# Kernel optimization log

Measured on AMD Instinct MI355X. Metric: run time of the kernel, lower is better.

## Reference

```python
import jax, jax.numpy as jnp
import numpy as np

EMBED_DIM = 1024
NUM_HEADS = 16
KEY_SIZE = 1024
VALUE_SIZE = 1024
N, L = 4, 2048


def setup_inputs() -> dict:
    key = jax.random.key(0)
    ks = jax.random.split(key, 8)
    s = lambda fan_in: 1.0 / np.sqrt(fan_in)
    return {
        "x": jax.random.normal(ks[0], (N, L, EMBED_DIM), dtype=jnp.float32),
        # nn.Linear weights stored as (out, in); we apply x @ W.T
        "W_q": jax.random.uniform(ks[1], (KEY_SIZE, EMBED_DIM), jnp.float32, -s(EMBED_DIM), s(EMBED_DIM)),
        "W_k": jax.random.uniform(ks[2], (KEY_SIZE, EMBED_DIM), jnp.float32, -s(EMBED_DIM), s(EMBED_DIM)),
        "W_v": jax.random.uniform(ks[3], (VALUE_SIZE, EMBED_DIM), jnp.float32, -s(EMBED_DIM), s(EMBED_DIM)),
        "W_qp": jax.random.uniform(ks[4], (KEY_SIZE, KEY_SIZE), jnp.float32, -s(KEY_SIZE), s(KEY_SIZE)),
        "W_kp": jax.random.uniform(ks[5], (KEY_SIZE, KEY_SIZE), jnp.float32, -s(KEY_SIZE), s(KEY_SIZE)),
        "W_vp": jax.random.uniform(ks[6], (VALUE_SIZE, VALUE_SIZE), jnp.float32, -s(VALUE_SIZE), s(VALUE_SIZE)),
        "W_out": jax.random.uniform(ks[7], (EMBED_DIM, VALUE_SIZE), jnp.float32, -s(VALUE_SIZE), s(VALUE_SIZE)),
    }


def reference(x, W_q, W_k, W_v, W_qp, W_kp, W_vp, W_out):
    H = NUM_HEADS
    q = (x @ W_q.T) @ W_qp.T   # (N, L, key_size)
    k = (x @ W_k.T) @ W_kp.T   # (N, L, key_size)
    v = (x @ W_v.T) @ W_vp.T   # (N, L, value_size)
    n, l, vs = v.shape
    dq = q.shape[-1] // H
    dv = vs // H
    q = q.reshape(n, l, H, dq).transpose(0, 2, 1, 3)  # (N, H, L, dq)
    k = k.reshape(n, l, H, dq).transpose(0, 2, 1, 3)
    v = v.reshape(n, l, H, dv).transpose(0, 2, 1, 3)
    att = jnp.einsum("nhid,nhjd->nhij", q, k) / jnp.sqrt(jnp.float32(dq))
    att = jax.nn.softmax(att, axis=-1)
    out = jnp.einsum("nhij,nhjd->nhid", att, v)       # (N, H, L, dv)
    out = out.transpose(0, 2, 1, 3).reshape(n, l, vs)
    return out @ W_out.T
```

## Files before the change

### kernel.cpp

```cpp
#include <hip/hip_runtime.h>
#include <cstddef>
#include <cstdint>

#define EMBED 1024
#define NH    16
#define DQ    64
#define NB    4
#define LSEQ  2048
#define MROWS (NB * LSEQ)

typedef __bf16 bf16x8 __attribute__((ext_vector_type(8)));
typedef float  f32x4  __attribute__((ext_vector_type(4)));

__device__ __forceinline__ unsigned short f2bf(float f) {
    return (unsigned short)((__float_as_uint(f) + 0x8000u) >> 16);
}

__device__ __forceinline__ unsigned pack2(float a, float b) {
    unsigned ua = __float_as_uint(a) + 0x8000u;
    unsigned ub = __float_as_uint(b) + 0x8000u;
    return __builtin_amdgcn_perm(ub, ua, 0x07060302u);
}

__device__ __forceinline__ uint2 pack4(float a, float b, float c, float d) {
    return make_uint2(pack2(a, b), pack2(c, d));
}

__device__ __forceinline__ unsigned pack2t(float a, float b) {
    return __builtin_amdgcn_perm(__float_as_uint(b), __float_as_uint(a), 0x07060302u);
}

__device__ __forceinline__ uint2 pack4t(float a, float b, float c, float d) {
    return make_uint2(pack2t(a, b), pack2t(c, d));
}

__device__ __forceinline__ void async_cp16(const void* g, void* l) {
    __builtin_amdgcn_global_load_lds((const __attribute__((address_space(1))) unsigned int*)g,
                                     (__attribute__((address_space(3))) unsigned int*)l,
                                     16, 0, 0);
}

struct CvtJobs {
    const float* src[8];
    unsigned short* dst[8];
    int n[8];
};

__global__ __launch_bounds__(256) void cvt_bf16(CvtJobs j) {
    int job = blockIdx.y;
    const float* s = j.src[job];
    unsigned short* d = j.dst[job];
    int n4 = j.n[job] >> 2;
    int stride = gridDim.x * blockDim.x;
    for (int i = blockIdx.x * blockDim.x + threadIdx.x; i < n4; i += stride) {
        float4 f = ((const float4*)s)[i];
        ((uint2*)d)[i] = pack4(f.x, f.y, f.z, f.w);
    }
}

struct TransJobs {
    const float* src[3];
    unsigned short* dst[3];
};

__global__ __launch_bounds__(256) void transpose_cvt(TransJobs tj) {
    __shared__ unsigned short Ts[64][68];
    const float* src = tj.src[blockIdx.z];
    unsigned short* dst = tj.dst[blockIdx.z];
    const int tid = threadIdx.x;
    const int r0 = blockIdx.y * 64;
    const int c0 = blockIdx.x * 64;

    {
        int col4 = tid & 15;
        int rb   = tid >> 4;
#pragma unroll
        for (int it = 0; it < 4; it++) {
            int r = rb + it * 16;
            float4 f = *(const float4*)(src + (size_t)(r0 + r) * 1024 + c0 + col4 * 4);
            *(uint2*)&Ts[r][col4 * 4] = pack4(f.x, f.y, f.z, f.w);
        }
    }
    __syncthreads();

    {
        int oc = tid >> 2;
        int seg = tid & 3;
        __attribute__((aligned(16))) unsigned short tmp[16];
#pragma unroll
        for (int e = 0; e < 16; e++) tmp[e] = Ts[seg * 16 + e][oc];
        unsigned short* out = dst + (size_t)(c0 + oc) * 1024 + r0 + seg * 16;
        *(uint4*)(out)     = *(const uint4*)&tmp[0];
        *(uint4*)(out + 8) = *(const uint4*)&tmp[8];
    }
}

struct BGemmArgs {
    const unsigned short* A[3];
    const unsigned short* B[3];
    void* C[3];
    int mode[3];
    float scl[3];
};

__global__ __launch_bounds__(256) void gemm_bf16nt(BGemmArgs p, int M, int N, int K) {
    __shared__ __align__(16) unsigned short As[128 * 64];
    __shared__ __align__(16) unsigned short Bs[128 * 64];

    const int tid  = threadIdx.x;
    const int wave = tid >> 6;
    const int lane = tid & 63;
    const int m16  = lane & 15;
    const int kq   = lane >> 4;
    const int bm = blockIdx.y * 128;
    const int bn = blockIdx.x * 128;
    const int z  = blockIdx.z;
    const unsigned short* A = p.A[z];
    const unsigned short* B = p.B[z];

    f32x4 acc[4][4];
#pragma unroll
    for (int i = 0; i < 4; i++)
#pragma unroll
        for (int j = 0; j < 4; j++) acc[i][j] = f32x4{0.f, 0.f, 0.f, 0.f};

    const int wr = (wave >> 1) * 64;
    const int wc = (wave & 1) * 64;

    for (int k0 = 0; k0 < K; k0 += 64) {
#pragma unroll
        for (int it = 0; it < 4; it++) {
            int c = tid + it * 256;
            int r = c >> 3;
            int kc = (c & 7) ^ (r & 7);
            async_cp16(A + (size_t)(bm + r) * K + k0 + kc * 8,
                       &As[(it * 256 + wave * 64) * 8]);
            async_cp16(B + (size_t)(bn + r) * K + k0 + kc * 8,
                       &Bs[(it * 256 + wave * 64) * 8]);
        }
        __syncthreads();

#pragma unroll
        for (int s = 0; s < 2; s++) {
            bf16x8 af[4], bfr[4];
#pragma unroll
            for (int i = 0; i < 4; i++) {
                int ra = wr + i * 16 + m16;
                af[i] = *reinterpret_cast<const bf16x8*>(
                    &As[ra * 64 + (((s * 4 + kq) ^ (ra & 7)) * 8)]);
                int rb = wc + i * 16 + m16;
                bfr[i] = *reinterpret_cast<const bf16x8*>(
                    &Bs[rb * 64 + (((s * 4 + kq) ^ (rb & 7)) * 8)]);
            }
#pragma unroll
            for (int i = 0; i < 4; i++)
#pragma unroll
                for (int j = 0; j < 4; j++)
                    acc[i][j] = __builtin_amdgcn_mfma_f32_16x16x32_bf16(af[i], bfr[j], acc[i][j], 0, 0, 0);
        }
        __syncthreads();
    }

    const int mode = p.mode[z];
    const float scl = p.scl[z];
    if (mode == 0) {
        unsigned short* Cb = (unsigned short*)p.C[z];
#pragma unroll
        for (int i = 0; i < 4; i++)
#pragma unroll
            for (int j = 0; j < 4; j++) {
                int row = bm + wr + i * 16 + kq * 4;
                int col = bn + wc + j * 16 + m16;
#pragma unroll
                for (int q = 0; q < 4; q++)
                    Cb[(size_t)(row + q) * N + col] = f2bf(acc[i][j][q] * scl);
            }
    } else if (mode == 1) {
        float* Cf = (float*)p.C[z];
#pragma unroll
        for (int i = 0; i < 4; i++)
#pragma unroll
            for (int j = 0; j < 4; j++) {
                int row = bm + wr + i * 16 + kq * 4;
                int col = bn + wc + j * 16 + m16;
#pragma unroll
                for (int q = 0; q < 4; q++)
                    Cf[(size_t)(row + q) * N + col] = acc[i][j][q];
            }
    } else {
        unsigned short* Ct = (unsigned short*)p.C[z];
#pragma unroll
        for (int i = 0; i < 4; i++)
#pragma unroll
            for (int j = 0; j < 4; j++) {
                int row = bm + wr + i * 16 + kq * 4;
                int col = bn + wc + j * 16 + m16;
                *reinterpret_cast<uint2*>(&Ct[(size_t)col * M + row]) =
                    pack4(acc[i][j][0], acc[i][j][1], acc[i][j][2], acc[i][j][3]);
            }
    }
}

__global__ __launch_bounds__(256, 4)
void flash_bf16(const unsigned short* __restrict__ qb,
                const unsigned short* __restrict__ kb,
                const unsigned short* __restrict__ vtb,
                unsigned short* __restrict__ ao) {
    __shared__ __align__(16) unsigned short Ks[64 * 64];
    __shared__ __align__(16) unsigned short Vt[64 * 64];
    __shared__ __align__(16) unsigned short Pt[4][32 * 40];

    const int tid  = threadIdx.x;
    const int wave = tid >> 6;
    const int lane = tid & 63;
    const int m16  = lane & 15;
    const int kq   = lane >> 4;
    const int nn = blockIdx.y >> 4;
    const int h  = blockIdx.y & 15;
    const int q0 = blockIdx.x * 128;

    const uint4 ones_u = make_uint4(0x3F803F80u, 0x3F803F80u, 0x3F803F80u, 0x3F803F80u);
    const bf16x8 av_ones = __builtin_bit_cast(bf16x8, ones_u);

    bf16x8 qf[2][2];
#pragma unroll
    for (int j = 0; j < 2; j++) {
        size_t tok = (size_t)(nn * LSEQ + q0 + wave * 32 + j * 16 + m16);
#pragma unroll
        for (int s = 0; s < 2; s++)
            qf[j][s] = *reinterpret_cast<const bf16x8*>(
                &qb[tok * EMBED + h * DQ + s * 32 + kq * 8]);
    }

    f32x4 o[4][2];
    f32x4 o4[2];
#pragma unroll
    for (int j = 0; j < 2; j++) {
        o4[j] = f32x4{0.f, 0.f, 0.f, 0.f};
#pragma unroll
        for (int mt = 0; mt < 4; mt++) o[mt][j] = f32x4{0.f, 0.f, 0.f, 0.f};
    }

    const unsigned short* kptr  = kb + (size_t)(nn * LSEQ) * EMBED + h * DQ;
    const unsigned short* vtptr = vtb + (size_t)(h * DQ) * MROWS + nn * LSEQ;

    for (int kt = 0; kt < LSEQ / 64; kt++) {
#pragma unroll
        for (int it = 0; it < 2; it++) {
            int c = tid + it * 256;
            int r = c >> 3;
            int kc = (c & 7) ^ (r & 7);
            async_cp16(kptr + (size_t)r * EMBED + kc * 8,
                       &Ks[(it * 256 + wave * 64) * 8]);
            async_cp16(vtptr + (size_t)r * MROWS + kc * 8,
                       &Vt[(it * 256 + wave * 64) * 8]);
        }
        kptr  += 64 * EMBED;
        vtptr += 64;
        __syncthreads();

        f32x4 st[4][2];
#pragma unroll
        for (int i = 0; i < 4; i++)
#pragma unroll
            for (int j = 0; j < 2; j++) st[i][j] = f32x4{0.f, 0.f, 0.f, 0.f};

#pragma unroll
        for (int s = 0; s < 2; s++) {
            bf16x8 ak[4];
#pragma unroll
            for (int i = 0; i < 4; i++) {
                int key = i * 16 + m16;
                ak[i] = *reinterpret_cast<const bf16x8*>(
                    &Ks[key * 64 + (((s * 4 + kq) ^ (m16 & 7)) * 8)]);
            }
#pragma unroll
            for (int i = 0; i < 4; i++)
#pragma unroll
                for (int j = 0; j < 2; j++)
                    st[i][j] = __builtin_amdgcn_mfma_f32_16x16x32_bf16(ak[i], qf[j][s], st[i][j], 0, 0, 0);
        }

#pragma unroll
        for (int i = 0; i < 4; i++)
#pragma unroll
            for (int j = 0; j < 2; j++)
#pragma unroll
                for (int q = 0; q < 4; q++)
                    st[i][j][q] = __builtin_amdgcn_exp2f(st[i][j][q]);

#pragma unroll
        for (int s = 0; s < 2; s++) {
#pragma unroll
            for (int i2 = 0; i2 < 2; i2++) {
                int i = s * 2 + i2;
#pragma unroll
                for (int j = 0; j < 2; j++)
                    *reinterpret_cast<uint2*>(
                        &Pt[wave][(j * 16 + m16) * 40 + i2 * 16 + kq * 4]) =
                        pack4t(st[i][j][0], st[i][j][1], st[i][j][2], st[i][j][3]);
            }
            bf16x8 av[4], bp[2];
#pragma unroll
            for (int mt = 0; mt < 4; mt++) {
                int d = mt * 16 + m16;
                av[mt] = *reinterpret_cast<const bf16x8*>(
                    &Vt[d * 64 + (((s * 4 + kq) ^ (m16 & 7)) * 8)]);
            }
#pragma unroll
            for (int j = 0; j < 2; j++)
                bp[j] = *reinterpret_cast<const bf16x8*>(
                    &Pt[wave][(j * 16 + m16) * 40 + kq * 8]);
#pragma unroll
            for (int mt = 0; mt < 4; mt++)
#pragma unroll
                for (int j = 0; j < 2; j++)
                    o[mt][j] = __builtin_amdgcn_mfma_f32_16x16x32_bf16(av[mt], bp[j], o[mt][j], 0, 0, 0);
#pragma unroll
            for (int j = 0; j < 2; j++)
                o4[j] = __builtin_amdgcn_mfma_f32_16x16x32_bf16(av_ones, bp[j], o4[j], 0, 0, 0);
        }
        __syncthreads();
    }

#pragma unroll
    for (int j = 0; j < 2; j++) {
        float inv = 1.f / o4[j][0];
        size_t tok = (size_t)(nn * LSEQ + q0 + wave * 32 + j * 16 + m16);
#pragma unroll
        for (int mt = 0; mt < 4; mt++) {
            *reinterpret_cast<uint2*>(&ao[tok * EMBED + h * DQ + mt * 16 + kq * 4]) =
                pack4(o[mt][j][0] * inv, o[mt][j][1] * inv, o[mt][j][2] * inv, o[mt][j][3] * inv);
        }
    }
}

extern "C" void kernel_launch(void* const* d_in, const int* in_sizes, int n_in,
                              void* d_out, int out_size, void* d_ws, size_t ws_size,
                              hipStream_t stream) {
    (void)in_sizes; (void)n_in; (void)out_size; (void)ws_size;
    const float* x     = (const float*)d_in[0];
    const float* W_q   = (const float*)d_in[1];
    const float* W_k   = (const float*)d_in[2];
    const float* W_v   = (const float*)d_in[3];
    const float* W_qp  = (const float*)d_in[4];
    const float* W_kp  = (const float*)d_in[5];
    const float* W_vp  = (const float*)d_in[6];
    const float* W_out = (const float*)d_in[7];

    unsigned short* ws16 = (unsigned short*)d_ws;
    const size_t SZX = (size_t)MROWS * EMBED;
    const size_t SZW = (size_t)EMBED * EMBED;

    unsigned short* xb    = ws16;
    unsigned short* wqpb  = xb + SZX;
    unsigned short* wkpb  = wqpb + SZW;
    unsigned short* wvpb  = wkpb + SZW;
    unsigned short* woutb = wvpb + SZW;
    unsigned short* wqT   = woutb + SZW;
    unsigned short* wkT   = wqT + SZW;
    unsigned short* wvT   = wkT + SZW;
    unsigned short* weq   = wvT + SZW;
    unsigned short* wek   = weq + SZW;
    unsigned short* wev   = wek + SZW;
    unsigned short* qbuf  = wev + SZW;
    unsigned short* kbuf  = qbuf + SZX;
    unsigned short* vtbuf = kbuf + SZX;
    unsigned short* ao    = vtbuf + SZX;

    CvtJobs cj;
    cj.src[0] = x;     cj.dst[0] = xb;    cj.n[0] = (int)SZX;
    cj.src[1] = W_qp;  cj.dst[1] = wqpb;  cj.n[1] = (int)SZW;
    cj.src[2] = W_kp;  cj.dst[2] = wkpb;  cj.n[2] = (int)SZW;
    cj.src[3] = W_vp;  cj.dst[3] = wvpb;  cj.n[3] = (int)SZW;
    cj.src[4] = W_out; cj.dst[4] = woutb; cj.n[4] = (int)SZW;
    cvt_bf16<<<dim3(512, 5), 256, 0, stream>>>(cj);

    TransJobs tj;
    tj.src[0] = W_q; tj.src[1] = W_k; tj.src[2] = W_v;
    tj.dst[0] = wqT; tj.dst[1] = wkT; tj.dst[2] = wvT;
    transpose_cvt<<<dim3(16, 16, 3), 256, 0, stream>>>(tj);

    BGemmArgs fz;
    fz.A[0] = wqpb; fz.A[1] = wkpb; fz.A[2] = wvpb;
    fz.B[0] = wqT;  fz.B[1] = wkT;  fz.B[2] = wvT;
    fz.C[0] = weq;  fz.C[1] = wek;  fz.C[2] = wev;
    fz.mode[0] = 0; fz.mode[1] = 0; fz.mode[2] = 0;
    fz.scl[0] = 1.f; fz.scl[1] = 1.f; fz.scl[2] = 1.f;
    gemm_bf16nt<<<dim3(8, 8, 3), 256, 0, stream>>>(fz, EMBED, EMBED, EMBED);

    BGemmArgs pj;
    pj.A[0] = xb;   pj.A[1] = xb;   pj.A[2] = xb;
    pj.B[0] = weq;  pj.B[1] = wek;  pj.B[2] = wev;
    pj.C[0] = qbuf; pj.C[1] = kbuf; pj.C[2] = vtbuf;
    pj.mode[0] = 0; pj.mode[1] = 0; pj.mode[2] = 2;
    pj.scl[0] = 0.18033688f; pj.scl[1] = 1.f; pj.scl[2] = 1.f;
    gemm_bf16nt<<<dim3(8, 64, 3), 256, 0, stream>>>(pj, MROWS, EMBED, EMBED);

    flash_bf16<<<dim3(LSEQ / 128, NB * NH), 256, 0, stream>>>(qbuf, kbuf, vtbuf, ao);

    BGemmArgs og;
    og.A[0] = ao;    og.A[1] = ao;    og.A[2] = ao;
    og.B[0] = woutb; og.B[1] = woutb; og.B[2] = woutb;
    og.C[0] = d_out; og.C[1] = d_out; og.C[2] = d_out;
    og.mode[0] = 1; og.mode[1] = 1; og.mode[2] = 1;
    og.scl[0] = 1.f; og.scl[1] = 1.f; og.scl[2] = 1.f;
    gemm_bf16nt<<<dim3(8, 64, 1), 256, 0, stream>>>(og, MROWS, EMBED, EMBED);
}
```

Measured before the change: 327.2 us.

## Double-buffer K/V tiles in flash kernel, swizzle blocks, stage V-transpose epilogue via LDS

```diff
diff --git a/kernel.cpp b/kernel.cpp
--- a/kernel.cpp
+++ b/kernel.cpp
@@ -104,8 +104,9 @@
 };
 
 __global__ __launch_bounds__(256) void gemm_bf16nt(BGemmArgs p, int M, int N, int K) {
-    __shared__ __align__(16) unsigned short As[128 * 64];
-    __shared__ __align__(16) unsigned short Bs[128 * 64];
+    __shared__ __align__(16) unsigned short SMEM[2 * 128 * 64];
+    unsigned short* As = SMEM;
+    unsigned short* Bs = SMEM + 128 * 64;
 
     const int tid  = threadIdx.x;
     const int wave = tid >> 6;
@@ -188,26 +189,39 @@
                     Cf[(size_t)(row + q) * N + col] = acc[i][j][q];
             }
     } else {
+        unsigned short* Tt = SMEM;
+#pragma unroll
+        for (int i = 0; i < 4; i++)
+#pragma unroll
+            for (int j = 0; j < 4; j++) {
+                int c = wc + j * 16 + m16;
+                int u = (wr >> 2) + i * 4 + kq;
+                int us = (u + 2 * c) & 31;
+                *reinterpret_cast<uint2*>(&Tt[c * 128 + us * 4]) =
+                    pack4(acc[i][j][0], acc[i][j][1], acc[i][j][2], acc[i][j][3]);
+            }
+        __syncthreads();
         unsigned short* Ct = (unsigned short*)p.C[z];
-#pragma unroll
-        for (int i = 0; i < 4; i++)
-#pragma unroll
-            for (int j = 0; j < 4; j++) {
-                int row = bm + wr + i * 16 + kq * 4;
-                int col = bn + wc + j * 16 + m16;
-                *reinterpret_cast<uint2*>(&Ct[(size_t)col * M + row]) =
-                    pack4(acc[i][j][0], acc[i][j][1], acc[i][j][2], acc[i][j][3]);
-            }
-    }
-}
-
-__global__ __launch_bounds__(256, 4)
+        int r8 = tid & 15;
+        int cb = tid >> 4;
+#pragma unroll
+        for (int pass = 0; pass < 8; pass++) {
+            int c  = pass * 16 + cb;
+            int u0 = r8 * 2;
+            int us = (u0 + 2 * c) & 31;
+            uint4 val = *reinterpret_cast<const uint4*>(&Tt[c * 128 + us * 4]);
+            *reinterpret_cast<uint4*>(&Ct[(size_t)(bn + c) * M + bm + r8 * 8]) = val;
+        }
+    }
+}
+
+__global__ __launch_bounds__(256, 3)
 void flash_bf16(const unsigned short* __restrict__ qb,
                 const unsigned short* __restrict__ kb,
                 const unsigned short* __restrict__ vtb,
                 unsigned short* __restrict__ ao) {
-    __shared__ __align__(16) unsigned short Ks[64 * 64];
-    __shared__ __align__(16) unsigned short Vt[64 * 64];
+    __shared__ __align__(16) unsigned short Ks[2][64 * 64];
+    __shared__ __align__(16) unsigned short Vt[2][64 * 64];
     __shared__ __align__(16) unsigned short Pt[4][32 * 40];
 
     const int tid  = threadIdx.x;
@@ -215,49 +229,68 @@
     const int lane = tid & 63;
     const int m16  = lane & 15;
     const int kq   = lane >> 4;
-    const int nn = blockIdx.y >> 4;
-    const int h  = blockIdx.y & 15;
-    const int q0 = blockIdx.x * 128;
+
+    const int flat = blockIdx.y * (LSEQ / 128) + blockIdx.x;
+    const int swz  = (flat & 7) * 128 + (flat >> 3);
+    const int bh   = swz >> 4;
+    const int nn   = bh >> 4;
+    const int h    = bh & 15;
+    const int q0   = (swz & 15) * 128;
 
     const uint4 ones_u = make_uint4(0x3F803F80u, 0x3F803F80u, 0x3F803F80u, 0x3F803F80u);
     const bf16x8 av_ones = __builtin_bit_cast(bf16x8, ones_u);
 
-    bf16x8 qf[2][2];
-#pragma unroll
-    for (int j = 0; j < 2; j++) {
-        size_t tok = (size_t)(nn * LSEQ + q0 + wave * 32 + j * 16 + m16);
-#pragma unroll
-        for (int s = 0; s < 2; s++)
-            qf[j][s] = *reinterpret_cast<const bf16x8*>(
-                &qb[tok * EMBED + h * DQ + s * 32 + kq * 8]);
-    }
-
-    f32x4 o[4][2];
-    f32x4 o4[2];
-#pragma unroll
-    for (int j = 0; j < 2; j++) {
-        o4[j] = f32x4{0.f, 0.f, 0.f, 0.f};
-#pragma unroll
-        for (int mt = 0; mt < 4; mt++) o[mt][j] = f32x4{0.f, 0.f, 0.f, 0.f};
-    }
-
     const unsigned short* kptr  = kb + (size_t)(nn * LSEQ) * EMBED + h * DQ;
     const unsigned short* vtptr = vtb + (size_t)(h * DQ) * MROWS + nn * LSEQ;
 
-    for (int kt = 0; kt < LSEQ / 64; kt++) {
+    auto stage = [&](int buf, const unsigned short* kp, const unsigned short* vp) {
 #pragma unroll
         for (int it = 0; it < 2; it++) {
             int c = tid + it * 256;
             int r = c >> 3;
             int kc = (c & 7) ^ (r & 7);
-            async_cp16(kptr + (size_t)r * EMBED + kc * 8,
-                       &Ks[(it * 256 + wave * 64) * 8]);
-            async_cp16(vtptr + (size_t)r * MROWS + kc * 8,
-                       &Vt[(it * 256 + wave * 64) * 8]);
-        }
-        kptr  += 64 * EMBED;
-        vtptr += 64;
-        __syncthreads();
+            async_cp16(kp + (size_t)r * EMBED + kc * 8,
+                       &Ks[buf][(it * 256 + wave * 64) * 8]);
+            async_cp16(vp + (size_t)r * MROWS + kc * 8,
+                       &Vt[buf][(it * 256 + wave * 64) * 8]);
+        }
+    };
+
+    stage(0, kptr, vtptr);
+    kptr  += 64 * EMBED;
+    vtptr += 64;
+
+    bf16x8 qf[2][2];
+#pragma unroll
+    for (int j = 0; j < 2; j++) {
+        size_t tok = (size_t)(nn * LSEQ + q0 + wave * 32 + j * 16 + m16);
+#pragma unroll
+        for (int s = 0; s < 2; s++)
+            qf[j][s] = *reinterpret_cast<const bf16x8*>(
+                &qb[tok * EMBED + h * DQ + s * 32 + kq * 8]);
+    }
+
+    f32x4 o[4][2];
+    f32x4 o4[2];
+#pragma unroll
+    for (int j = 0; j < 2; j++) {
+        o4[j] = f32x4{0.f, 0.f, 0.f, 0.f};
+#pragma unroll
+        for (int mt = 0; mt < 4; mt++) o[mt][j] = f32x4{0.f, 0.f, 0.f, 0.f};
+    }
+
+    asm volatile("s_waitcnt vmcnt(0)" ::: "memory");
+    __builtin_amdgcn_s_barrier();
+    asm volatile("" ::: "memory");
+
+    const int NT = LSEQ / 64;
+    for (int kt = 0; kt < NT; kt++) {
+        const int cur = kt & 1;
+        if (kt + 1 < NT) {
+            stage(cur ^ 1, kptr, vtptr);
+            kptr  += 64 * EMBED;
+            vtptr += 64;
+        }
 
         f32x4 st[4][2];
 #pragma unroll
@@ -272,7 +305,7 @@
             for (int i = 0; i < 4; i++) {
                 int key = i * 16 + m16;
                 ak[i] = *reinterpret_cast<const bf16x8*>(
-                    &Ks[key * 64 + (((s * 4 + kq) ^ (m16 & 7)) * 8)]);
+                    &Ks[cur][key * 64 + (((s * 4 + kq) ^ (m16 & 7)) * 8)]);
             }
 #pragma unroll
             for (int i = 0; i < 4; i++)
@@ -305,7 +338,7 @@
             for (int mt = 0; mt < 4; mt++) {
                 int d = mt * 16 + m16;
                 av[mt] = *reinterpret_cast<const bf16x8*>(
-                    &Vt[d * 64 + (((s * 4 + kq) ^ (m16 & 7)) * 8)]);
+                    &Vt[cur][d * 64 + (((s * 4 + kq) ^ (m16 & 7)) * 8)]);
             }
 #pragma unroll
             for (int j = 0; j < 2; j++)
@@ -320,7 +353,10 @@
             for (int j = 0; j < 2; j++)
                 o4[j] = __builtin_amdgcn_mfma_f32_16x16x32_bf16(av_ones, bp[j], o4[j], 0, 0, 0);
         }
-        __syncthreads();
+
+        asm volatile("s_waitcnt vmcnt(0) lgkmcnt(0)" ::: "memory");
+        __builtin_amdgcn_s_barrier();
+        asm volatile("" ::: "memory");
     }
 
 #pragma unroll
@@ -401,8 +437,8 @@
 
     BGemmArgs og;
     og.A[0] = ao;    og.A[1] = ao;    og.A[2] = ao;
+    og.C[0] = d_out; og.C[1] = d_out; og.C[2] = d_out;
     og.B[0] = woutb; og.B[1] = woutb; og.B[2] = woutb;
-    og.C[0] = d_out; og.C[1] = d_out; og.C[2] = d_out;
     og.mode[0] = 1; og.mode[1] = 1; og.mode[2] = 1;
     og.scl[0] = 1.f; og.scl[1] = 1.f; og.scl[2] = 1.f;
     gemm_bf16nt<<<dim3(8, 64, 1), 256, 0, stream>>>(og, MROWS, EMBED, EMBED);
```

Measured after the change: 325.9 us. No clear change (-0.4%).

## Swizzle workgroup order for XCD locality and stage transposed GEMM stores through LDS

Applied to the files above, without the earlier changes.

```diff
diff --git a/kernel.cpp b/kernel.cpp
--- a/kernel.cpp
+++ b/kernel.cpp
@@ -104,16 +104,21 @@
 };
 
 __global__ __launch_bounds__(256) void gemm_bf16nt(BGemmArgs p, int M, int N, int K) {
-    __shared__ __align__(16) unsigned short As[128 * 64];
-    __shared__ __align__(16) unsigned short Bs[128 * 64];
+    __shared__ __align__(16) unsigned short SMEM[2 * 128 * 64];
+    unsigned short* As = SMEM;
+    unsigned short* Bs = SMEM + 128 * 64;
 
     const int tid  = threadIdx.x;
     const int wave = tid >> 6;
     const int lane = tid & 63;
     const int m16  = lane & 15;
     const int kq   = lane >> 4;
-    const int bm = blockIdx.y * 128;
-    const int bn = blockIdx.x * 128;
+
+    const int nwg  = gridDim.x * gridDim.y;
+    const int flat = blockIdx.y * gridDim.x + blockIdx.x;
+    const int swz  = (flat & 7) * (nwg >> 3) + (flat >> 3);
+    const int bm = (swz / gridDim.x) * 128;
+    const int bn = (swz % gridDim.x) * 128;
     const int z  = blockIdx.z;
     const unsigned short* A = p.A[z];
     const unsigned short* B = p.B[z];
@@ -188,16 +193,29 @@
                     Cf[(size_t)(row + q) * N + col] = acc[i][j][q];
             }
     } else {
+        unsigned short* Tt = SMEM;
+#pragma unroll
+        for (int i = 0; i < 4; i++)
+#pragma unroll
+            for (int j = 0; j < 4; j++) {
+                int c = wc + j * 16 + m16;
+                int u = (wr >> 2) + i * 4 + kq;
+                int us = (u + 2 * c) & 31;
+                *reinterpret_cast<uint2*>(&Tt[c * 128 + us * 4]) =
+                    pack4(acc[i][j][0], acc[i][j][1], acc[i][j][2], acc[i][j][3]);
+            }
+        __syncthreads();
         unsigned short* Ct = (unsigned short*)p.C[z];
-#pragma unroll
-        for (int i = 0; i < 4; i++)
-#pragma unroll
-            for (int j = 0; j < 4; j++) {
-                int row = bm + wr + i * 16 + kq * 4;
-                int col = bn + wc + j * 16 + m16;
-                *reinterpret_cast<uint2*>(&Ct[(size_t)col * M + row]) =
-                    pack4(acc[i][j][0], acc[i][j][1], acc[i][j][2], acc[i][j][3]);
-            }
+        int r8 = tid & 15;
+        int cb = tid >> 4;
+#pragma unroll
+        for (int pass = 0; pass < 8; pass++) {
+            int c  = pass * 16 + cb;
+            int u0 = r8 * 2;
+            int us = (u0 + 2 * c) & 31;
+            uint4 val = *reinterpret_cast<const uint4*>(&Tt[c * 128 + us * 4]);
+            *reinterpret_cast<uint4*>(&Ct[(size_t)(bn + c) * M + bm + r8 * 8]) = val;
+        }
     }
 }
 
@@ -215,9 +233,13 @@
     const int lane = tid & 63;
     const int m16  = lane & 15;
     const int kq   = lane >> 4;
-    const int nn = blockIdx.y >> 4;
-    const int h  = blockIdx.y & 15;
-    const int q0 = blockIdx.x * 128;
+
+    const int flat = blockIdx.y * (LSEQ / 128) + blockIdx.x;
+    const int swz  = (flat & 7) * 128 + (flat >> 3);
+    const int bh   = swz >> 4;
+    const int nn   = bh >> 4;
+    const int h    = bh & 15;
+    const int q0   = (swz & 15) * 128;
 
     const uint4 ones_u = make_uint4(0x3F803F80u, 0x3F803F80u, 0x3F803F80u, 0x3F803F80u);
     const bf16x8 av_ones = __builtin_bit_cast(bf16x8, ones_u);
```

After: 305.2 us. 6.7% less time.
